# Kernel optimization log

Hardware: AMD Instinct MI355X
Metric: run time of the kernel (lower is better)

The kernel has to match this reference:

```python
import jax, jax.numpy as jnp
import numpy as np

B, S, D, H = 2, 2048, 1024, 16


def setup_inputs() -> dict:
    key = jax.random.key(0)
    kq, kk, kv, kw = jax.random.split(key, 4)
    Q = jax.random.normal(kq, (B, S, D), dtype=jnp.float32)
    K = jax.random.normal(kk, (B, S, D), dtype=jnp.float32)
    V = jax.random.normal(kv, (B, S, D), dtype=jnp.float32)
    Wo = jax.random.normal(kw, (D, D), dtype=jnp.float32) * (1.0 / np.sqrt(D))
    return {"Q": Q, "K": K, "V": V, "Wo": Wo, "num_heads": H}


def reference(Q, K, V, Wo, num_heads):
    b, s, d = Q.shape
    dk = d // num_heads
    # split heads: [B,S,D] -> [B,H,S,dk]
    q = Q.reshape(b, s, num_heads, dk).transpose(0, 2, 1, 3)
    k = K.reshape(b, s, num_heads, dk).transpose(0, 2, 1, 3)
    v = V.reshape(b, s, num_heads, dk).transpose(0, 2, 1, 3)
    scale = 1.0 / jnp.sqrt(jnp.asarray(dk, dtype=q.dtype))
    logits = jnp.einsum('bhqd,bhkd->bhqk', q, k) * scale  # [B,H,S,S]
    probs = jax.nn.softmax(logits, axis=-1).astype(q.dtype)
    o = jnp.einsum('bhqk,bhkd->bhqd', probs, v)  # [B,H,S,dk]
    o = o.transpose(0, 2, 1, 3).reshape(b, s, d)  # concat heads
    # O = einsum('d dkh, ... dkh -> ... d', Wo, scores) == scores @ Wo^T
    return jnp.einsum('dk,bsk->bsd', Wo, o)
```

## Files before the change

kernel.cpp:

```cpp
#include <hip/hip_runtime.h>
#include <hip/hip_bf16.h>

#define B_ 2
#define S_ 2048
#define D_ 1024
#define H_ 16
#define DK_ 64

typedef __hip_bfloat16 bf16;
typedef short v8s __attribute__((ext_vector_type(8)));
typedef short v4s __attribute__((ext_vector_type(4)));
typedef float v4f __attribute__((ext_vector_type(4)));
typedef float v16f __attribute__((ext_vector_type(16)));
typedef int   v4i __attribute__((ext_vector_type(4)));
typedef int   v2i __attribute__((ext_vector_type(2)));

static __device__ __forceinline__ v16f mfma32(v8s a, v8s b, v16f c) {
  return __builtin_amdgcn_mfma_f32_32x32x16_bf16(a, b, c, 0, 0, 0);
}
static __device__ __forceinline__ void gl2lds16(const void* g, void* l) {
  __builtin_amdgcn_global_load_lds((const __attribute__((address_space(1))) void*)g,
                                   (__attribute__((address_space(3))) void*)l,
                                   16, 0, 0);
}
static __device__ __forceinline__ short f2bf(float x) {
  return (short)__builtin_bit_cast(unsigned short, __float2bfloat16(x));
}
static __device__ __forceinline__ int pk2f(float lo, float hi) {
  unsigned a = __builtin_bit_cast(unsigned, lo) + 0x8000u;
  unsigned b = __builtin_bit_cast(unsigned, hi) + 0x8000u;
  return (int)__builtin_amdgcn_perm(b, a, 0x07060302u);
}
static __device__ __forceinline__ float bf2f(short s) {
  return __builtin_bit_cast(float, ((unsigned)(unsigned short)s) << 16);
}

__global__ __launch_bounds__(256) void pre_kernel(
    const float* __restrict__ K, const float* __restrict__ V,
    const float* __restrict__ Wo, bf16* __restrict__ Kb,
    bf16* __restrict__ Vt, bf16* __restrict__ Wb)
{
  __shared__ __align__(16) bf16 td[64 * 72];
  const int t = threadIdx.x;
  const int bx = blockIdx.x;

  if (bx < 2048) {
    const int idx = bx * 256 + t;
    const int seg = idx & 7;
    const int rest = idx >> 3;
    const int h = rest & 15;
    const int bs = rest >> 4;
    const float* src = K + (size_t)bs * D_ + h * 64 + seg * 8;
    v4f x = *(const v4f*)src, y = *(const v4f*)(src + 4);
    v8s r;
    r[0]=f2bf(x[0]); r[1]=f2bf(x[1]); r[2]=f2bf(x[2]); r[3]=f2bf(x[3]);
    r[4]=f2bf(y[0]); r[5]=f2bf(y[1]); r[6]=f2bf(y[2]); r[7]=f2bf(y[3]);
    const int b = bs >> 11, s = bs & 2047;
    *(v8s*)(Kb + ((size_t)(b * H_ + h) * S_ + s) * DK_ + seg * 8) = r;
  } else if (bx < 3072) {
    const int idx = bx - 2048;
    const int bh = idx >> 5, b = bh >> 4, h = bh & 15;
    const int s0 = (idx & 31) * 64;
    const int srow = t >> 2;
    const int cs = t & 3;
    const float* vp = V + (size_t)(b * S_ + s0 + srow) * D_ + h * 64 + cs * 16;
#pragma unroll
    for (int j = 0; j < 4; j++) {
      v4f x = *(const v4f*)(vp + j * 4);
#pragma unroll
      for (int jj = 0; jj < 4; jj++)
        td[(cs * 16 + j * 4 + jj) * 72 + srow] = __float2bfloat16(x[jj]);
    }
    __syncthreads();
    const int d = t >> 2;
#pragma unroll
    for (int a2 = 0; a2 < 4; a2++) {
      const int pos = cs * 16 + a2 * 4;
      const int g = pos >> 5;
      const int a = (pos >> 2) & 7;
      const int kbase = g * 32 + ((a >> 2) << 4) + ((a & 1) << 3) + (((a >> 1) & 1) << 2);
      v4s val = *(const v4s*)(td + d * 72 + kbase);
      *(v4s*)(Vt + ((size_t)bh * DK_ + d) * S_ + s0 + pos) = val;
    }
  } else {
    const int i = ((bx - 3072) * 256 + t) * 4;
    v4f a = *(const v4f*)(Wo + i);
    v4s r;
    r[0]=f2bf(a[0]); r[1]=f2bf(a[1]); r[2]=f2bf(a[2]); r[3]=f2bf(a[3]);
    *(v4s*)((short*)Wb + i) = r;
  }
}

__global__ __launch_bounds__(256, 4) void attn4_kernel(
    const float* __restrict__ Q, const bf16* __restrict__ Kb,
    const bf16* __restrict__ Vt, bf16* __restrict__ Op0,
    bf16* __restrict__ Op1, float* __restrict__ Lp)
{
  __shared__ __align__(16) bf16 kk[2][64 * 64];
  __shared__ __align__(16) bf16 vv[2][64 * 64];

  const int t = threadIdx.x;
  const int w = t >> 6, l = t & 63, h2 = l >> 5, ln = l & 31;

  const int bid = blockIdx.x;
  const int xcd = bid & 7;
  const int idx = bid >> 3;
  const int bh  = xcd * 4 + (idx >> 5);
  const int rest = idx & 31;
  const int qt = rest & 15, z = rest >> 4;

  const int b = bh >> 4, h = bh & 15;
  const int qbase = qt * 128 + w * 32;
  const int kb0 = z << 10;

  const bf16* Kbh = Kb + (size_t)bh * (S_ * DK_);
  const bf16* Vbh = Vt + (size_t)bh * (DK_ * S_);

  const float sc = 0.18033688011112042f;
  v8s bq[4];
  {
    const float* qp = Q + ((size_t)b * S_ + qbase + ln) * D_ + h * DK_ + h2 * 8;
#pragma unroll
    for (int c = 0; c < 4; c++) {
      v4f x = *(const v4f*)(qp + c * 16);
      v4f y = *(const v4f*)(qp + c * 16 + 4);
      v4i r = { pk2f(x[0]*sc, x[1]*sc), pk2f(x[2]*sc, x[3]*sc),
                pk2f(y[0]*sc, y[1]*sc), pk2f(y[2]*sc, y[3]*sc) };
      bq[c] = __builtin_bit_cast(v8s, r);
    }
  }

  v16f Z;
#pragma unroll
  for (int r = 0; r < 16; r++) Z[r] = 0.f;

  v16f accA, accB;
#pragma unroll
  for (int r = 0; r < 16; r++) { accA[r] = 0.f; accB[r] = 0.f; }
  float lpart = 0.f;

#pragma unroll
  for (int j = 0; j < 2; j++) {
    const int flat = j * 256 + t, row = flat >> 3, sp = flat & 7;
    gl2lds16(Kbh + (size_t)(kb0 + row) * DK_ + ((sp ^ (row & 7)) * 8), &kk[0][flat * 8]);
    gl2lds16(Vbh + (size_t)row * S_ + kb0 + ((sp ^ (row & 7)) * 8), &vv[0][flat * 8]);
  }

  int it = 0;
  for (int kb = kb0; kb < kb0 + 1024; kb += 64, it ^= 1) {
    __syncthreads();
    if (kb + 64 < kb0 + 1024) {
#pragma unroll
      for (int j = 0; j < 2; j++) {
        const int flat = j * 256 + t, row = flat >> 3, sp = flat & 7;
        gl2lds16(Kbh + (size_t)(kb + 64 + row) * DK_ + ((sp ^ (row & 7)) * 8),
                 &kk[it ^ 1][flat * 8]);
        gl2lds16(Vbh + (size_t)row * S_ + (kb + 64) + ((sp ^ (row & 7)) * 8),
                 &vv[it ^ 1][flat * 8]);
      }
    }
    const bf16* kc_ = kk[it];
    const bf16* vc_ = vv[it];

    v16f s0, s1;
    __builtin_amdgcn_s_setprio(1);
#pragma unroll
    for (int c = 0; c < 4; c++) {
      const int sd = 2 * c + h2;
      v8s a0 = *(const v8s*)(kc_ + ln * 64 + ((sd ^ (ln & 7)) * 8));
      v8s a1 = *(const v8s*)(kc_ + (32 + ln) * 64 + ((sd ^ (ln & 7)) * 8));
      if (c == 0) {
        s0 = mfma32(a0, bq[0], Z);
        s1 = mfma32(a1, bq[0], Z);
      } else {
        s0 = mfma32(a0, bq[c], s0);
        s1 = mfma32(a1, bq[c], s1);
      }
    }
    __builtin_amdgcn_s_setprio(0);

    float p0[16], p1[16];
#pragma unroll
    for (int r = 0; r < 16; r++) { p0[r] = exp2f(s0[r]); p1[r] = exp2f(s1[r]); }
    float suA = 0.f, suB = 0.f;
#pragma unroll
    for (int r = 0; r < 16; r++) { suA += p0[r]; suB += p1[r]; }
    lpart += suA + suB;

    v4i i00 = { pk2f(p0[0],p0[1]),  pk2f(p0[2],p0[3]),  pk2f(p0[4],p0[5]),  pk2f(p0[6],p0[7]) };
    v4i i01 = { pk2f(p0[8],p0[9]),  pk2f(p0[10],p0[11]),pk2f(p0[12],p0[13]),pk2f(p0[14],p0[15]) };
    v4i i10 = { pk2f(p1[0],p1[1]),  pk2f(p1[2],p1[3]),  pk2f(p1[4],p1[5]),  pk2f(p1[6],p1[7]) };
    v4i i11 = { pk2f(p1[8],p1[9]),  pk2f(p1[10],p1[11]),pk2f(p1[12],p1[13]),pk2f(p1[14],p1[15]) };
    v8s pb00 = __builtin_bit_cast(v8s, i00);
    v8s pb01 = __builtin_bit_cast(v8s, i01);
    v8s pb10 = __builtin_bit_cast(v8s, i10);
    v8s pb11 = __builtin_bit_cast(v8s, i11);

    __builtin_amdgcn_s_setprio(1);
#pragma unroll
    for (int st = 0; st < 2; st++) {
#pragma unroll
      for (int kc = 0; kc < 2; kc++) {
        const int q = st * 4 + kc * 2 + h2;
        v8s avA = *(const v8s*)(vc_ + ln * 64 + ((q ^ (ln & 7)) * 8));
        v8s avB = *(const v8s*)(vc_ + (32 + ln) * 64 + ((q ^ (ln & 7)) * 8));
        v8s pb = st ? (kc ? pb11 : pb10) : (kc ? pb01 : pb00);
        accA = mfma32(avA, pb, accA);
        accB = mfma32(avB, pb, accB);
      }
    }
    __builtin_amdgcn_s_setprio(0);
  }

  __syncthreads();
  const float lfull = lpart + __shfl_xor(lpart, 32);
  bf16* epw = &kk[0][0] + w * 2048;
#pragma unroll
  for (int r = 0; r < 16; r += 4) {
    const int off = 4 * h2;
    const int sgA = (r >> 2) ^ (ln & 3);
    const int sgB = 4 + sgA;
    v2i pa = { pk2f(accA[r],   accA[r+1]),
               pk2f(accA[r+2], accA[r+3]) };
    v2i pb = { pk2f(accB[r],   accB[r+1]),
               pk2f(accB[r+2], accB[r+3]) };
    *(v2i*)(epw + ln * 64 + sgA * 8 + off) = pa;
    *(v2i*)(epw + ln * 64 + sgB * 8 + off) = pb;
  }
  if (h2 == 0)
    Lp[((size_t)z * 32 + bh) * S_ + qbase + ln] = lfull;

  bf16* Op = z ? Op1 : Op0;
#pragma unroll
  for (int i = 0; i < 4; i++) {
    const int flat = i * 64 + l;
    const int qr = flat >> 3, sd = flat & 7;
    const int phys = ((sd & 3) ^ (qr & 3)) | (sd & 4);
    v8s val = *(const v8s*)(epw - w * 2048 + (w * 32 + qr) * 64 + phys * 8);
    *(v8s*)(Op + ((size_t)b * S_ + qbase - w * 32 + w * 32 + qr) * D_ + h * DK_ + sd * 8) = val;
  }
}

__global__ __launch_bounds__(256) void merge_kernel(
    const bf16* __restrict__ Op0, const bf16* __restrict__ Op1,
    const float* __restrict__ Lp, bf16* __restrict__ O)
{
  const int flat = blockIdx.x * 256 + threadIdx.x;
  const int qrow = flat >> 7;
  const int seg = flat & 127;
  const int b = qrow >> 11, s = qrow & 2047;
  const int h = seg >> 3;
  const int bh = b * H_ + h;
  const float l0 = Lp[(size_t)bh * S_ + s];
  const float l1 = Lp[(size_t)(32 + bh) * S_ + s];
  const float inv = 1.0f / (l0 + l1);
  const size_t off = (size_t)qrow * D_ + seg * 8;
  v8s a = *(const v8s*)(Op0 + off);
  v8s c = *(const v8s*)(Op1 + off);
  v4i r;
#pragma unroll
  for (int j = 0; j < 4; j++) {
    float lo = (bf2f(a[2*j])   + bf2f(c[2*j]))   * inv;
    float hi = (bf2f(a[2*j+1]) + bf2f(c[2*j+1])) * inv;
    r[j] = pk2f(lo, hi);
  }
  *(v8s*)(O + off) = __builtin_bit_cast(v8s, r);
}

__global__ __launch_bounds__(512, 1) void projm_kernel(
    const bf16* __restrict__ A, const bf16* __restrict__ Wo, float* __restrict__ Out)
{
  __shared__ __align__(16) bf16 aa[2][128 * 64];
  __shared__ __align__(16) bf16 bb[2][128 * 64];

  const int t = threadIdx.x;
  const int w = t >> 6, l = t & 63, h2 = l >> 5, ln = l & 31;
  const int m0 = blockIdx.x * 128, n0 = blockIdx.y * 128;
  const int wm = (w & 3) * 32;
  const int wn = (w >> 2) * 64;

  v16f acc0, acc1;
#pragma unroll
  for (int r = 0; r < 16; r++) { acc0[r] = 0.f; acc1[r] = 0.f; }

  auto stage = [&](int k0, int buf) {
#pragma unroll
    for (int j = 0; j < 2; j++) {
      const int flat = j * 512 + t, row = flat >> 3, sp = flat & 7;
      gl2lds16(A  + (size_t)(m0 + row) * D_ + k0 + ((sp ^ (row & 7)) * 8),
               &aa[buf][flat * 8]);
      gl2lds16(Wo + (size_t)(n0 + row) * D_ + k0 + ((sp ^ (row & 7)) * 8),
               &bb[buf][flat * 8]);
    }
  };

  stage(0, 0);

  int it = 0;
  for (int k0 = 0; k0 < D_; k0 += 64, it ^= 1) {
    __syncthreads();
    if (k0 + 64 < D_) stage(k0 + 64, it ^ 1);
    const bf16* ac = aa[it];
    const bf16* bc = bb[it];
#pragma unroll
    for (int c = 0; c < 4; c++) {
      const int sd = 2 * c + h2;
      const int x0 = (sd ^ (ln & 7)) * 8;
      v8s a  = *(const v8s*)(ac + (wm + ln) * 64 + x0);
      v8s b0 = *(const v8s*)(bc + (wn + ln) * 64 + x0);
      v8s b1 = *(const v8s*)(bc + (wn + 32 + ln) * 64 + x0);
      acc0 = mfma32(a, b0, acc0);
      acc1 = mfma32(a, b1, acc1);
    }
  }

#pragma unroll
  for (int r = 0; r < 16; r++) {
    const int rr = (r & 3) + 4 * h2 + 8 * (r >> 2);
    float* o = Out + (size_t)(m0 + wm + rr) * D_ + n0 + wn;
    o[ln]      = acc0[r];
    o[32 + ln] = acc1[r];
  }
}

extern "C" void kernel_launch(void* const* d_in, const int* in_sizes, int n_in,
                              void* d_out, int out_size, void* d_ws, size_t ws_size,
                              hipStream_t stream) {
  (void)in_sizes; (void)n_in; (void)out_size; (void)ws_size;
  const float* Q  = (const float*)d_in[0];
  const float* K  = (const float*)d_in[1];
  const float* V  = (const float*)d_in[2];
  const float* Wo = (const float*)d_in[3];
  float* out = (float*)d_out;

  bf16* base = (bf16*)d_ws;
  bf16* kb   = base;
  bf16* vt   = base + (size_t)4  * 1024 * 1024;
  bf16* wo_b = base + (size_t)8  * 1024 * 1024;
  bf16* op0  = base + (size_t)9  * 1024 * 1024;
  bf16* op1  = base + (size_t)13 * 1024 * 1024;
  float* lp  = (float*)(base + (size_t)17 * 1024 * 1024);
  bf16* ows  = kb;

  pre_kernel  <<<dim3(4096),       256, 0, stream>>>(K, V, Wo, kb, vt, wo_b);
  attn4_kernel<<<dim3(1024),       256, 0, stream>>>(Q, kb, vt, op0, op1, lp);
  merge_kernel<<<dim3(2048),       256, 0, stream>>>(op0, op1, lp, ows);
  projm_kernel<<<dim3(32, 8),      512, 0, stream>>>(ows, wo_b, out);
}
```

Before: 176.7 us.

## Drop split-K attention and merge kernel; normalize in attention epilogue

```diff
diff --git a/kernel.cpp b/kernel.cpp
--- a/kernel.cpp
+++ b/kernel.cpp
@@ -73,15 +73,20 @@
     }
     __syncthreads();
     const int d = t >> 2;
+    v4s g_[4];
 #pragma unroll
     for (int a2 = 0; a2 < 4; a2++) {
       const int pos = cs * 16 + a2 * 4;
       const int g = pos >> 5;
       const int a = (pos >> 2) & 7;
       const int kbase = g * 32 + ((a >> 2) << 4) + ((a & 1) << 3) + (((a >> 1) & 1) << 2);
-      v4s val = *(const v4s*)(td + d * 72 + kbase);
-      *(v4s*)(Vt + ((size_t)bh * DK_ + d) * S_ + s0 + pos) = val;
-    }
+      g_[a2] = *(const v4s*)(td + d * 72 + kbase);
+    }
+    v8s w0 = { g_[0][0],g_[0][1],g_[0][2],g_[0][3], g_[1][0],g_[1][1],g_[1][2],g_[1][3] };
+    v8s w1 = { g_[2][0],g_[2][1],g_[2][2],g_[2][3], g_[3][0],g_[3][1],g_[3][2],g_[3][3] };
+    bf16* dst = Vt + ((size_t)bh * DK_ + d) * S_ + s0 + cs * 16;
+    *(v8s*)(dst)     = w0;
+    *(v8s*)(dst + 8) = w1;
   } else {
     const int i = ((bx - 3072) * 256 + t) * 4;
     v4f a = *(const v4f*)(Wo + i);
@@ -93,8 +98,7 @@
 
 __global__ __launch_bounds__(256, 4) void attn4_kernel(
     const float* __restrict__ Q, const bf16* __restrict__ Kb,
-    const bf16* __restrict__ Vt, bf16* __restrict__ Op0,
-    bf16* __restrict__ Op1, float* __restrict__ Lp)
+    const bf16* __restrict__ Vt, bf16* __restrict__ O)
 {
   __shared__ __align__(16) bf16 kk[2][64 * 64];
   __shared__ __align__(16) bf16 vv[2][64 * 64];
@@ -105,13 +109,11 @@
   const int bid = blockIdx.x;
   const int xcd = bid & 7;
   const int idx = bid >> 3;
-  const int bh  = xcd * 4 + (idx >> 5);
-  const int rest = idx & 31;
-  const int qt = rest & 15, z = rest >> 4;
+  const int bh  = xcd * 4 + (idx >> 4);
+  const int qt  = idx & 15;
 
   const int b = bh >> 4, h = bh & 15;
   const int qbase = qt * 128 + w * 32;
-  const int kb0 = z << 10;
 
   const bf16* Kbh = Kb + (size_t)bh * (S_ * DK_);
   const bf16* Vbh = Vt + (size_t)bh * (DK_ * S_);
@@ -142,14 +144,14 @@
 #pragma unroll
   for (int j = 0; j < 2; j++) {
     const int flat = j * 256 + t, row = flat >> 3, sp = flat & 7;
-    gl2lds16(Kbh + (size_t)(kb0 + row) * DK_ + ((sp ^ (row & 7)) * 8), &kk[0][flat * 8]);
-    gl2lds16(Vbh + (size_t)row * S_ + kb0 + ((sp ^ (row & 7)) * 8), &vv[0][flat * 8]);
+    gl2lds16(Kbh + (size_t)row * DK_ + ((sp ^ (row & 7)) * 8), &kk[0][flat * 8]);
+    gl2lds16(Vbh + (size_t)row * S_ + ((sp ^ (row & 7)) * 8), &vv[0][flat * 8]);
   }
 
   int it = 0;
-  for (int kb = kb0; kb < kb0 + 1024; kb += 64, it ^= 1) {
+  for (int kb = 0; kb < S_; kb += 64, it ^= 1) {
     __syncthreads();
-    if (kb + 64 < kb0 + 1024) {
+    if (kb + 64 < S_) {
 #pragma unroll
       for (int j = 0; j < 2; j++) {
         const int flat = j * 256 + t, row = flat >> 3, sp = flat & 7;
@@ -214,57 +216,29 @@
 
   __syncthreads();
   const float lfull = lpart + __shfl_xor(lpart, 32);
+  const float linv = 1.0f / lfull;
   bf16* epw = &kk[0][0] + w * 2048;
 #pragma unroll
   for (int r = 0; r < 16; r += 4) {
     const int off = 4 * h2;
     const int sgA = (r >> 2) ^ (ln & 3);
     const int sgB = 4 + sgA;
-    v2i pa = { pk2f(accA[r],   accA[r+1]),
-               pk2f(accA[r+2], accA[r+3]) };
-    v2i pb = { pk2f(accB[r],   accB[r+1]),
-               pk2f(accB[r+2], accB[r+3]) };
+    v2i pa = { pk2f(accA[r]*linv,   accA[r+1]*linv),
+               pk2f(accA[r+2]*linv, accA[r+3]*linv) };
+    v2i pb = { pk2f(accB[r]*linv,   accB[r+1]*linv),
+               pk2f(accB[r+2]*linv, accB[r+3]*linv) };
     *(v2i*)(epw + ln * 64 + sgA * 8 + off) = pa;
     *(v2i*)(epw + ln * 64 + sgB * 8 + off) = pb;
   }
-  if (h2 == 0)
-    Lp[((size_t)z * 32 + bh) * S_ + qbase + ln] = lfull;
-
-  bf16* Op = z ? Op1 : Op0;
+  __syncthreads();
 #pragma unroll
   for (int i = 0; i < 4; i++) {
     const int flat = i * 64 + l;
     const int qr = flat >> 3, sd = flat & 7;
     const int phys = ((sd & 3) ^ (qr & 3)) | (sd & 4);
     v8s val = *(const v8s*)(epw - w * 2048 + (w * 32 + qr) * 64 + phys * 8);
-    *(v8s*)(Op + ((size_t)b * S_ + qbase - w * 32 + w * 32 + qr) * D_ + h * DK_ + sd * 8) = val;
-  }
-}
-
-__global__ __launch_bounds__(256) void merge_kernel(
-    const bf16* __restrict__ Op0, const bf16* __restrict__ Op1,
-    const float* __restrict__ Lp, bf16* __restrict__ O)
-{
-  const int flat = blockIdx.x * 256 + threadIdx.x;
-  const int qrow = flat >> 7;
-  const int seg = flat & 127;
-  const int b = qrow >> 11, s = qrow & 2047;
-  const int h = seg >> 3;
-  const int bh = b * H_ + h;
-  const float l0 = Lp[(size_t)bh * S_ + s];
-  const float l1 = Lp[(size_t)(32 + bh) * S_ + s];
-  const float inv = 1.0f / (l0 + l1);
-  const size_t off = (size_t)qrow * D_ + seg * 8;
-  v8s a = *(const v8s*)(Op0 + off);
-  v8s c = *(const v8s*)(Op1 + off);
-  v4i r;
-#pragma unroll
-  for (int j = 0; j < 4; j++) {
-    float lo = (bf2f(a[2*j])   + bf2f(c[2*j]))   * inv;
-    float hi = (bf2f(a[2*j+1]) + bf2f(c[2*j+1])) * inv;
-    r[j] = pk2f(lo, hi);
-  }
-  *(v8s*)(O + off) = __builtin_bit_cast(v8s, r);
+    *(v8s*)(O + ((size_t)b * S_ + qbase + qr) * D_ + h * DK_ + sd * 8) = val;
+  }
 }
 
 __global__ __launch_bounds__(512, 1) void projm_kernel(
@@ -337,13 +311,9 @@
   bf16* kb   = base;
   bf16* vt   = base + (size_t)4  * 1024 * 1024;
   bf16* wo_b = base + (size_t)8  * 1024 * 1024;
-  bf16* op0  = base + (size_t)9  * 1024 * 1024;
-  bf16* op1  = base + (size_t)13 * 1024 * 1024;
-  float* lp  = (float*)(base + (size_t)17 * 1024 * 1024);
-  bf16* ows  = kb;
-
-  pre_kernel  <<<dim3(4096),       256, 0, stream>>>(K, V, Wo, kb, vt, wo_b);
-  attn4_kernel<<<dim3(1024),       256, 0, stream>>>(Q, kb, vt, op0, op1, lp);
-  merge_kernel<<<dim3(2048),       256, 0, stream>>>(op0, op1, lp, ows);
-  projm_kernel<<<dim3(32, 8),      512, 0, stream>>>(ows, wo_b, out);
-}
+  bf16* ows  = base + (size_t)9  * 1024 * 1024;
+
+  pre_kernel  <<<dim3(4096),   256, 0, stream>>>(K, V, Wo, kb, vt, wo_b);
+  attn4_kernel<<<dim3(512),    256, 0, stream>>>(Q, kb, vt, ows);
+  projm_kernel<<<dim3(32, 8),  512, 0, stream>>>(ows, wo_b, out);
+}
```

New measurement: 176.0 us. About the same (-0.4%).

## Use 8-wave attention blocks with 256-query tiles sharing each K/V stage

Applied to the files above, without the earlier changes.

```diff
diff --git a/kernel.cpp b/kernel.cpp
--- a/kernel.cpp
+++ b/kernel.cpp
@@ -73,15 +73,20 @@
     }
     __syncthreads();
     const int d = t >> 2;
+    v4s g_[4];
 #pragma unroll
     for (int a2 = 0; a2 < 4; a2++) {
       const int pos = cs * 16 + a2 * 4;
       const int g = pos >> 5;
       const int a = (pos >> 2) & 7;
       const int kbase = g * 32 + ((a >> 2) << 4) + ((a & 1) << 3) + (((a >> 1) & 1) << 2);
-      v4s val = *(const v4s*)(td + d * 72 + kbase);
-      *(v4s*)(Vt + ((size_t)bh * DK_ + d) * S_ + s0 + pos) = val;
-    }
+      g_[a2] = *(const v4s*)(td + d * 72 + kbase);
+    }
+    v8s w0 = { g_[0][0],g_[0][1],g_[0][2],g_[0][3], g_[1][0],g_[1][1],g_[1][2],g_[1][3] };
+    v8s w1 = { g_[2][0],g_[2][1],g_[2][2],g_[2][3], g_[3][0],g_[3][1],g_[3][2],g_[3][3] };
+    bf16* dst = Vt + ((size_t)bh * DK_ + d) * S_ + s0 + cs * 16;
+    *(v8s*)(dst)     = w0;
+    *(v8s*)(dst + 8) = w1;
   } else {
     const int i = ((bx - 3072) * 256 + t) * 4;
     v4f a = *(const v4f*)(Wo + i);
@@ -91,13 +96,12 @@
   }
 }
 
-__global__ __launch_bounds__(256, 4) void attn4_kernel(
+__global__ __launch_bounds__(512, 4) void attn8_kernel(
     const float* __restrict__ Q, const bf16* __restrict__ Kb,
     const bf16* __restrict__ Vt, bf16* __restrict__ Op0,
     bf16* __restrict__ Op1, float* __restrict__ Lp)
 {
-  __shared__ __align__(16) bf16 kk[2][64 * 64];
-  __shared__ __align__(16) bf16 vv[2][64 * 64];
+  __shared__ __align__(16) bf16 smem[16384];
 
   const int t = threadIdx.x;
   const int w = t >> 6, l = t & 63, h2 = l >> 5, ln = l & 31;
@@ -105,12 +109,12 @@
   const int bid = blockIdx.x;
   const int xcd = bid & 7;
   const int idx = bid >> 3;
-  const int bh  = xcd * 4 + (idx >> 5);
-  const int rest = idx & 31;
-  const int qt = rest & 15, z = rest >> 4;
+  const int bh  = xcd * 4 + (idx >> 4);
+  const int rest = idx & 15;
+  const int qt = rest & 7, z = rest >> 3;
 
   const int b = bh >> 4, h = bh & 15;
-  const int qbase = qt * 128 + w * 32;
+  const int qbase = qt * 256 + w * 32;
   const int kb0 = z << 10;
 
   const bf16* Kbh = Kb + (size_t)bh * (S_ * DK_);
@@ -139,28 +143,23 @@
   for (int r = 0; r < 16; r++) { accA[r] = 0.f; accB[r] = 0.f; }
   float lpart = 0.f;
 
-#pragma unroll
-  for (int j = 0; j < 2; j++) {
-    const int flat = j * 256 + t, row = flat >> 3, sp = flat & 7;
-    gl2lds16(Kbh + (size_t)(kb0 + row) * DK_ + ((sp ^ (row & 7)) * 8), &kk[0][flat * 8]);
-    gl2lds16(Vbh + (size_t)row * S_ + kb0 + ((sp ^ (row & 7)) * 8), &vv[0][flat * 8]);
-  }
+  const int srow = t >> 3, ssp = t & 7;
+  const int soff = ((ssp ^ (srow & 7)) * 8);
+
+  gl2lds16(Kbh + (size_t)(kb0 + srow) * DK_ + soff, smem + t * 8);
+  gl2lds16(Vbh + (size_t)srow * S_ + kb0 + soff, smem + 8192 + t * 8);
 
   int it = 0;
   for (int kb = kb0; kb < kb0 + 1024; kb += 64, it ^= 1) {
     __syncthreads();
     if (kb + 64 < kb0 + 1024) {
-#pragma unroll
-      for (int j = 0; j < 2; j++) {
-        const int flat = j * 256 + t, row = flat >> 3, sp = flat & 7;
-        gl2lds16(Kbh + (size_t)(kb + 64 + row) * DK_ + ((sp ^ (row & 7)) * 8),
-                 &kk[it ^ 1][flat * 8]);
-        gl2lds16(Vbh + (size_t)row * S_ + (kb + 64) + ((sp ^ (row & 7)) * 8),
-                 &vv[it ^ 1][flat * 8]);
-      }
-    }
-    const bf16* kc_ = kk[it];
-    const bf16* vc_ = vv[it];
+      gl2lds16(Kbh + (size_t)(kb + 64 + srow) * DK_ + soff,
+               smem + (it ^ 1) * 4096 + t * 8);
+      gl2lds16(Vbh + (size_t)srow * S_ + (kb + 64) + soff,
+               smem + 8192 + (it ^ 1) * 4096 + t * 8);
+    }
+    const bf16* kc_ = smem + it * 4096;
+    const bf16* vc_ = smem + 8192 + it * 4096;
 
     v16f s0, s1;
     __builtin_amdgcn_s_setprio(1);
@@ -214,7 +213,7 @@
 
   __syncthreads();
   const float lfull = lpart + __shfl_xor(lpart, 32);
-  bf16* epw = &kk[0][0] + w * 2048;
+  bf16* epw = smem + w * 2048;
 #pragma unroll
   for (int r = 0; r < 16; r += 4) {
     const int off = 4 * h2;
@@ -236,8 +235,8 @@
     const int flat = i * 64 + l;
     const int qr = flat >> 3, sd = flat & 7;
     const int phys = ((sd & 3) ^ (qr & 3)) | (sd & 4);
-    v8s val = *(const v8s*)(epw - w * 2048 + (w * 32 + qr) * 64 + phys * 8);
-    *(v8s*)(Op + ((size_t)b * S_ + qbase - w * 32 + w * 32 + qr) * D_ + h * DK_ + sd * 8) = val;
+    v8s val = *(const v8s*)(epw + qr * 64 + phys * 8);
+    *(v8s*)(Op + ((size_t)b * S_ + qbase + qr) * D_ + h * DK_ + sd * 8) = val;
   }
 }
 
@@ -342,8 +341,8 @@
   float* lp  = (float*)(base + (size_t)17 * 1024 * 1024);
   bf16* ows  = kb;
 
-  pre_kernel  <<<dim3(4096),       256, 0, stream>>>(K, V, Wo, kb, vt, wo_b);
-  attn4_kernel<<<dim3(1024),       256, 0, stream>>>(Q, kb, vt, op0, op1, lp);
-  merge_kernel<<<dim3(2048),       256, 0, stream>>>(op0, op1, lp, ows);
-  projm_kernel<<<dim3(32, 8),      512, 0, stream>>>(ows, wo_b, out);
-}
+  pre_kernel  <<<dim3(4096),   256, 0, stream>>>(K, V, Wo, kb, vt, wo_b);
+  attn8_kernel<<<dim3(512),    512, 0, stream>>>(Q, kb, vt, op0, op1, lp);
+  merge_kernel<<<dim3(2048),   256, 0, stream>>>(op0, op1, lp, ows);
+  projm_kernel<<<dim3(32, 8),  512, 0, stream>>>(ows, wo_b, out);
+}
```

Result: no change. 176.3 us (-0.2%).
